# Optimization experiments

Measured on AMD Instinct MI355X. Metric: run time of the kernel, lower is better.

## Reference

```python
import jax, jax.numpy as jnp
import numpy as np

N_NEG = 60
TEMP = 0.07

def _normalize(x, axis):
    n = jnp.sqrt(jnp.sum(x * x, axis=axis, keepdims=True))
    return x / jnp.maximum(n, 1e-12)

def _grid_sample(img, grid):
    # img [B,C,H,W], grid [B,h,w,2] in [-1,1]; bilinear, padding_mode='border', align_corners=False
    B, C, H, W = img.shape
    ix = jnp.clip((grid[..., 0] + 1.0) * (W * 0.5) - 0.5, 0.0, W - 1.0)
    iy = jnp.clip((grid[..., 1] + 1.0) * (H * 0.5) - 0.5, 0.0, H - 1.0)
    x0 = jnp.floor(ix); y0 = jnp.floor(iy)
    x1 = jnp.minimum(x0 + 1.0, W - 1.0); y1 = jnp.minimum(y0 + 1.0, H - 1.0)
    wx = (ix - x0)[:, None]; wy = (iy - y0)[:, None]  # [B,1,h,w]
    imgf = img.reshape(B, C, H * W)
    hh, ww = grid.shape[1], grid.shape[2]
    def gat(yy, xx):
        idx = (yy * W + xx).astype(jnp.int32).reshape(B, 1, hh * ww)
        return jnp.take_along_axis(imgf, idx, axis=2).reshape(B, C, hh, ww)
    v00 = gat(y0, x0); v01 = gat(y0, x1); v10 = gat(y1, x0); v11 = gat(y1, x1)
    return (v00 * (1 - wx) * (1 - wy) + v01 * wx * (1 - wy)
            + v10 * (1 - wx) * wy + v11 * wx * wy)

def _forward(ref_fms, tgt_fms, target_l, target_r, queue):
    b, c, h, w = ref_fms.shape
    s = target_l.shape[-1] // w  # integer downscale factor (nearest interpolate == strided slice)
    disps_l = target_l[:, :, ::s, ::s] / float(s)   # [b,1,h,w]
    disps_r = target_r[:, :, ::s, ::s] / float(s)
    xb = jnp.broadcast_to(jnp.linspace(0.0, 1.0, w), (b, h, w))
    yb = jnp.broadcast_to(jnp.linspace(0.0, 1.0, h)[:, None], (b, h, w))

    def warp(img, disp):
        g = jnp.stack([xb + disp[:, 0] / w, yb], axis=-1)
        return _grid_sample(img, 2.0 * g - 1.0)

    # occlusion / validity mask (detached in the original)
    index = jnp.broadcast_to(jnp.arange(w, dtype=ref_fms.dtype), (b, 1, h, w))
    l2r2l = warp(warp(index, disps_r), -disps_l)
    masko = jnp.abs(index - l2r2l)[:, 0] < 3.0
    mask = masko & (disps_l[:, 0] > 0.0) & (xb - disps_l[:, 0] / w >= 0.0)
    mask = jax.lax.stop_gradient(mask).astype(ref_fms.dtype)  # [b,h,w]

    query = _normalize(ref_fms, 1)
    # positive: warp right feature to left view via disparity
    gpos = jnp.stack([xb - disps_l[:, 0] / w, yb], axis=-1)
    positive = _normalize(_grid_sample(tgt_fms, 2.0 * gpos - 1.0), 1)
    l_pos = jnp.einsum('bchw,bchw->bhw', query, positive)[..., None]

    # negatives: random integer pixel shifts around positive location
    # (no n_neg-fold repeat of tgt_fms; vmap grid_sample over the n axis instead)
    k1, k2 = jax.random.split(jax.random.key(1234))
    mag = jax.random.randint(k1, (b, h, w, N_NEG), 1, 25).astype(ref_fms.dtype)
    sgn = jnp.sign(jax.random.uniform(k2, (b, h, w, N_NEG)) - 0.5).astype(ref_fms.dtype)
    x_right = (xb - disps_l[:, 0] / w) * w
    fx = jnp.mod(x_right[..., None] + mag * sgn, float(w)) / w
    fy = fx / h  # faithful to original code (y coord reuses the normalized x coord)
    grids = jnp.moveaxis(jnp.stack([fx, fy], axis=-1), 3, 0)  # [n,b,h,w,2]
    neg = jax.vmap(lambda g: _grid_sample(tgt_fms, 2.0 * g - 1.0))(grids)  # [n,b,c,h,w]
    neg = _normalize(jnp.moveaxis(neg, 0, -1), 1)  # [b,c,h,w,n]
    l_neg = jnp.einsum('bchw,bchwn->bhwn', query, neg)

    qn = _normalize(queue, 0)  # forward re-normalizes the queue each call
    l_q = jnp.einsum('bchw,ck->bhwk', query, jax.lax.stop_gradient(qn))

    logits = jnp.concatenate([l_pos, l_neg, l_q], axis=-1) * mask[..., None]
    logits = logits.reshape(b * h * w, -1) / TEMP
    # CrossEntropyLoss with all-zero labels (positive is class 0)
    return jnp.mean(-jax.nn.log_softmax(logits, axis=-1)[:, 0])

def setup_inputs():
    key = jax.random.key(0)
    k1, k2, k3, k4, k5 = jax.random.split(key, 5)
    b, c, h, w = 2, 128, 64, 128
    H, W = 4 * h, 4 * w
    return {
        'ref_fms': jax.random.normal(k1, (b, c, h, w), jnp.float32),
        'tgt_fms': jax.random.normal(k2, (b, c, h, w), jnp.float32),
        'target_l': jax.random.uniform(k3, (b, 1, H, W), jnp.float32) * 64.0,
        'target_r': jax.random.uniform(k4, (b, 1, H, W), jnp.float32) * 64.0,
        'queue': jax.random.normal(k5, (c, 6000), jnp.float32),
    }

def reference(ref_fms, tgt_fms, target_l, target_r, queue):
    return _forward(ref_fms, tgt_fms, target_l, target_r, queue)
```

## Files before the change

### kernel.cpp

```cpp
#include <hip/hip_runtime.h>
#include <stdint.h>
#include <math.h>

#define HFM 64
#define WFM 128
#define CFM 128
#define BN 2
#define HWFM (HFM*WFM)
#define NPIX (BN*HWFM)
#define KQ 6000
#define KQP 6144
#define NNEG 60
#define NE (NPIX*NNEG)
#define EHALF_U 491520u
#define MSHIFT 15.0f
#define LOG2E 1.4426950408889634f
#define BSTRIDE 136

typedef _Float16 f16_8 __attribute__((ext_vector_type(8)));
typedef _Float16 f16_2 __attribute__((ext_vector_type(2)));
typedef float f32_4 __attribute__((ext_vector_type(4)));

__host__ __device__ __forceinline__ void threefry2x32(uint32_t k0, uint32_t k1,
                                                      uint32_t x0, uint32_t x1,
                                                      uint32_t* o0, uint32_t* o1) {
  uint32_t ks2 = k0 ^ k1 ^ 0x1BD11BDAu;
  x0 += k0; x1 += k1;
#define TFR(r) { x0 += x1; x1 = (x1 << (r)) | (x1 >> (32 - (r))); x1 ^= x0; }
  TFR(13) TFR(15) TFR(26) TFR(6)
  x0 += k1;  x1 += ks2 + 1u;
  TFR(17) TFR(29) TFR(16) TFR(24)
  x0 += ks2; x1 += k0 + 2u;
  TFR(13) TFR(15) TFR(26) TFR(6)
  x0 += k0;  x1 += k1 + 3u;
  TFR(17) TFR(29) TFR(16) TFR(24)
  x0 += k1;  x1 += ks2 + 4u;
  TFR(13) TFR(15) TFR(26) TFR(6)
  x0 += ks2; x1 += k0 + 5u;
#undef TFR
  *o0 = x0; *o1 = x1;
}

__device__ __forceinline__ void gs_coord(float t, float halfdim, float maxc,
                                         int* i0, int* i1, float* w) {
  float g = 2.0f * t - 1.0f;
  float x = (g + 1.0f) * halfdim - 0.5f;
  x = fminf(fmaxf(x, 0.0f), maxc);
  float f = floorf(x);
  *i0 = (int)f;
  *w = x - f;
  *i1 = (int)fminf(f + 1.0f, maxc);
}

__global__ __launch_bounds__(256) void k_A(
    const float* __restrict__ ref, const float* __restrict__ tgt,
    const float* __restrict__ queue,
    const float* __restrict__ target_l, const float* __restrict__ target_r,
    _Float16* __restrict__ refTf, _Float16* __restrict__ tgtTf,
    _Float16* __restrict__ queueTf, float2* __restrict__ qeb,
    float* __restrict__ maskArr, float* __restrict__ xr) {
  __shared__ float tile[32][33];
  int blk = blockIdx.x;
  int tid = threadIdx.x;
  if (blk < 64) {
    int p = blk * 256 + tid;
    int b = p >> 13;
    int rem = p & (HWFM - 1);
    int i = rem >> 7, j = rem & 127;
    const float stepx = 1.0f / 127.0f, stepy = 1.0f / 63.0f;
    float xb = (j == 127) ? 1.0f : j * stepx;
    float yb = (i == 63) ? 1.0f : i * stepy;
    const float* tl = target_l + (size_t)b * 256 * 512;
    const float* tr = target_r + (size_t)b * 256 * 512;
    float dl = tl[(4 * i) * 512 + 4 * j] * 0.25f;
    int y0i, y1i; float wy;
    gs_coord(yb, 32.0f, 63.0f, &y0i, &y1i, &wy);
    float t = xb - dl * (1.0f / 128.0f);
    int x0i, x1i; float wx;
    gs_coord(t, 64.0f, 127.0f, &x0i, &x1i, &wx);
    auto innerv = [&](int y, int x) -> float {
      float xbx = (x == 127) ? 1.0f : x * stepx;
      float drv = tr[(4 * y) * 512 + 4 * x] * 0.25f;
      float ti = xbx + drv * (1.0f / 128.0f);
      float g = 2.0f * ti - 1.0f;
      float ix2 = fminf(fmaxf((g + 1.0f) * 64.0f - 0.5f, 0.0f), 127.0f);
      float x0f = floorf(ix2);
      float wxp = ix2 - x0f;
      float x1f = fminf(x0f + 1.0f, 127.0f);
      return x0f * (1.0f - wxp) + x1f * wxp;
    };
    float v00 = innerv(y0i, x0i), v01 = innerv(y0i, x1i);
    float v10 = innerv(y1i, x0i), v11 = innerv(y1i, x1i);
    float l2r2l = v00 * (1.0f - wx) * (1.0f - wy) + v01 * wx * (1.0f - wy)
                + v10 * (1.0f - wx) * wy + v11 * wx * wy;
    bool masko = fabsf((float)j - l2r2l) < 3.0f;
    bool mk = masko && (dl > 0.0f) && (t >= 0.0f);
    maskArr[p] = mk ? 1.0f : 0.0f;
    xr[p] = t * 128.0f;
  } else if (blk < 88) {
    int k = (blk - 64) * 256 + tid;
    if (k < KQP) {
      if (k >= KQ) { qeb[k] = make_float2(0.0f, -1000.0f); }
      else {
        float ss = 0.0f;
        for (int c = 0; c < CFM; c++) { float v = queue[c * KQ + k]; ss += v * v; }
        float qi = 1.0f / fmaxf(sqrtf(ss), 1e-12f);
        qeb[k] = make_float2(qi * (LOG2E / 0.07f), -MSHIFT * LOG2E);
      }
    }
  } else if (blk < 856) {
    int q = blk - 88;
    int cy = q / 192, nx = q - cy * 192;
    int n0 = nx * 32, c0 = cy * 32;
    int tx = tid & 31, ty = tid >> 5;
#pragma unroll
    for (int i = 0; i < 32; i += 8) {
      int n = n0 + tx;
      tile[ty + i][tx] = (n < KQ) ? queue[(size_t)(c0 + ty + i) * KQ + n] : 0.0f;
    }
    __syncthreads();
#pragma unroll
    for (int i = 0; i < 32; i += 8)
      queueTf[(size_t)(n0 + ty + i) * CFM + (c0 + tx)] = (_Float16)tile[tx][ty + i];
  } else {
    int fblk = blk - 856;
    int z = fblk >> 10, yb_ = (fblk >> 8) & 3, xb_ = fblk & 255;
    int arr = z >> 1, b = z & 1;
    const float* src = (arr == 0 ? ref : tgt) + (size_t)b * CFM * HWFM;
    _Float16* dst = (arr == 0 ? refTf : tgtTf) + (size_t)b * HWFM * CFM;
    int x0 = xb_ * 32, y0 = yb_ * 32;
    int tx = tid & 31, ty = tid >> 5;
#pragma unroll
    for (int i = 0; i < 32; i += 8)
      tile[ty + i][tx] = src[(size_t)(y0 + ty + i) * HWFM + x0 + tx];
    __syncthreads();
#pragma unroll
    for (int i = 0; i < 32; i += 8)
      dst[(size_t)(x0 + ty + i) * CFM + (y0 + tx)] = (_Float16)tile[tx][ty + i];
  }
}

__global__ __launch_bounds__(256) void k_B(
    const _Float16* __restrict__ refTf, const _Float16* __restrict__ tgtTf,
    _Float16* __restrict__ QTf, float* __restrict__ stats,
    const float* __restrict__ maskArr, const float* __restrict__ xr,
    float* __restrict__ S, float* __restrict__ logit0,
    int* __restrict__ count, int* __restrict__ list) {
  __shared__ int wsum[4];
  int blk = blockIdx.x;
  int tid = threadIdx.x;
  int lane = tid & 63;
  if (blk == 0) {
    int wave = tid >> 6;
    int base_p = tid * 64;
    unsigned long long bits = 0ull;
    const float4* m4 = (const float4*)(maskArr + base_p);
#pragma unroll
    for (int k = 0; k < 16; k++) {
      float4 v = m4[k];
      if (v.x > 0.0f) bits |= 1ull << (4 * k + 0);
      if (v.y > 0.0f) bits |= 1ull << (4 * k + 1);
      if (v.z > 0.0f) bits |= 1ull << (4 * k + 2);
      if (v.w > 0.0f) bits |= 1ull << (4 * k + 3);
    }
    int m = __popcll(bits);
    int scan = m;
#pragma unroll
    for (int off = 1; off < 64; off <<= 1) {
      int n = __shfl_up(scan, off, 64);
      if (lane >= off) scan += n;
    }
    if (lane == 63) wsum[wave] = scan;
    __syncthreads();
    int wbase = 0;
    for (int w = 0; w < wave; w++) wbase += wsum[w];
    int idx = wbase + scan - m;
    for (int k = 0; k < 64; k++) {
      if ((bits >> k) & 1ull) list[idx++] = base_p + k;
    }
    if (tid == 255) *count = idx;
  } else if (blk < 65) {
    int sub = tid >> 6;
    int xg = (blk - 1) * 4 + sub;
    int b = xg >> 7, x = xg & 127;
    int xp = min(x + 1, 127);
    int c2 = lane * 2;
    int base = b * HWFM;
    f16_2 c0  = *(const f16_2*)(tgtTf + (size_t)(base + x) * CFM + c2);
    f16_2 c1  = *(const f16_2*)(tgtTf + (size_t)(base + WFM + x) * CFM + c2);
    f16_2 c0p = *(const f16_2*)(tgtTf + (size_t)(base + xp) * CFM + c2);
    f16_2 c1p = *(const f16_2*)(tgtTf + (size_t)(base + WFM + xp) * CFM + c2);
    float a0 = (float)c0[0], a1 = (float)c0[1];
    float b0 = (float)c1[0], b1 = (float)c1[1];
    float p0 = (float)c0p[0], p1 = (float)c0p[1];
    float q0 = (float)c1p[0], q1 = (float)c1p[1];
    float s[7];
    s[0] = a0 * a0 + a1 * a1;
    s[1] = a0 * b0 + a1 * b1;
    s[2] = b0 * b0 + b1 * b1;
    s[3] = a0 * p0 + a1 * p1;
    s[4] = a0 * q0 + a1 * q1;
    s[5] = b0 * p0 + b1 * p1;
    s[6] = b0 * q0 + b1 * q1;
#pragma unroll
    for (int o = 32; o; o >>= 1)
#pragma unroll
      for (int k = 0; k < 7; k++) s[k] += __shfl_xor(s[k], o, 64);
    if (lane == 0) {
      float* st = stats + (size_t)xg * 8;
#pragma unroll
      for (int k = 0; k < 7; k++) st[k] = s[k];
      st[7] = 0.0f;
    }
  } else {
    int wave = tid >> 6;
    int p = (blk - 65) * 4 + wave;
    float mk = maskArr[p];
    if (mk == 0.0f) return;
    int b = p >> 13;
    int rem = p & (HWFM - 1);
    int i = rem >> 7;
    const float stepy = 1.0f / 63.0f;
    float yb = (i == 63) ? 1.0f : i * stepy;
    float t = xr[p] * (1.0f / 128.0f);
    int y0i, y1i; float wy;
    gs_coord(yb, 32.0f, 63.0f, &y0i, &y1i, &wy);
    int x0i, x1i; float wx;
    gs_coord(t, 64.0f, 127.0f, &x0i, &x1i, &wx);

    int c2 = lane * 2;
    f16_2 q2 = *(const f16_2*)(refTf + (size_t)p * CFM + c2);
    int bo = b * HWFM;
    f16_2 a2 = *(const f16_2*)(tgtTf + (size_t)(bo + y0i * WFM + x0i) * CFM + c2);
    f16_2 b2 = *(const f16_2*)(tgtTf + (size_t)(bo + y0i * WFM + x1i) * CFM + c2);
    f16_2 cc2 = *(const f16_2*)(tgtTf + (size_t)(bo + y1i * WFM + x0i) * CFM + c2);
    f16_2 d2 = *(const f16_2*)(tgtTf + (size_t)(bo + y1i * WFM + x1i) * CFM + c2);

    float w00 = (1.0f - wx) * (1.0f - wy), w01 = wx * (1.0f - wy);
    float w10 = (1.0f - wx) * wy,          w11 = wx * wy;
    float q0 = (float)q2[0], q1 = (float)q2[1];
    float v0 = w00 * (float)a2[0] + w01 * (float)b2[0] + w10 * (float)cc2[0] + w11 * (float)d2[0];
    float v1 = w00 * (float)a2[1] + w01 * (float)b2[1] + w10 * (float)cc2[1] + w11 * (float)d2[1];

    float s0 = q0 * q0 + q1 * q1;
    float s1 = q0 * v0 + q1 * v1;
    float s2 = v0 * v0 + v1 * v1;
#pragma unroll
    for (int o = 32; o; o >>= 1) {
      s0 += __shfl_xor(s0, o, 64);
      s1 += __shfl_xor(s1, o, 64);
      s2 += __shfl_xor(s2, o, 64);
    }
    float inv = 1.0f / fmaxf(sqrtf(s0), 1e-12f);
    f16_2 qw; qw[0] = (_Float16)(q0 * inv); qw[1] = (_Float16)(q1 * inv);
    *(f16_2*)(QTf + (size_t)p * CFM + c2) = qw;
    if (lane == 0) {
      float lpos = (s1 * inv) / fmaxf(sqrtf(s2), 1e-12f);
      float lg0 = lpos / 0.07f;
      logit0[p] = lg0;
      S[p] = expf(lg0 - MSHIFT);
    }
  }
}

__global__ __launch_bounds__(256) void k_gemm(
    const _Float16* __restrict__ QTf,
    const _Float16* __restrict__ queueTf,
    const _Float16* __restrict__ tgtTf,
    const float2* __restrict__ qeb,
    float* __restrict__ S, float* __restrict__ D,
    const int* __restrict__ count, const int* __restrict__ list) {
  __shared__ _Float16 Bs[2][128 * BSTRIDE];
  __shared__ float Srow[64];
  __shared__ int pb[64];
  int tid = threadIdx.x;
  int cnt = *count;
  int pblk = blockIdx.y * 64;
  if (pblk >= cnt) return;
  int wave = tid >> 6, lane = tid & 63;
  int quad = lane >> 4, l16 = lane & 15;
  int wm = wave >> 1, wn = wave & 1;

  if (tid < 64) {
    Srow[tid] = 0.0f;
    pb[tid] = list[min(pblk + tid, cnt - 1)] >> 13;
  }

  f16_8 Af[2][4];
  int r0 = pblk + wm * 32;
#pragma unroll
  for (int mt = 0; mt < 2; mt++) {
    int prow = list[min(r0 + mt * 16 + l16, cnt - 1)];
    const _Float16* arow = QTf + (size_t)prow * CFM + quad * 8;
#pragma unroll
    for (int ks = 0; ks < 4; ks++)
      Af[mt][ks] = *(const f16_8*)(arow + ks * 32);
  }

  f16_8 sreg[8];
  int srow[8], sc16[8];
#pragma unroll
  for (int it = 0; it < 8; it++) {
    int idx = it * 256 + tid;
    srow[it] = idx >> 4; sc16[it] = idx & 15;
  }
  auto load_src = [&](const _Float16* bsrc) {
#pragma unroll
    for (int it = 0; it < 8; it++)
      sreg[it] = *(const f16_8*)(bsrc + (size_t)srow[it] * CFM + sc16[it] * 8);
  };
  auto write_lds = [&](int buf) {
#pragma unroll
    for (int it = 0; it < 8; it++)
      *(f16_8*)(&Bs[buf][srow[it] * BSTRIDE + sc16[it] * 8]) = sreg[it];
  };

  int nbase = blockIdx.x * 8 * 128;
  int cur;
  float rowsum[2][4] = {{0.0f,0.0f,0.0f,0.0f},{0.0f,0.0f,0.0f,0.0f}};

  if (blockIdx.x < 4) {
    int batch = blockIdx.x >> 1;
    load_src(tgtTf + ((size_t)batch * HWFM + (blockIdx.x & 1) * 128) * CFM);
    write_lds(0);
    __syncthreads();
    load_src(queueTf + (size_t)nbase * CFM);
    f32_4 acc[2][4];
#pragma unroll
    for (int mt = 0; mt < 2; mt++)
#pragma unroll
      for (int nt = 0; nt < 4; nt++)
        acc[mt][nt] = (f32_4){0.0f, 0.0f, 0.0f, 0.0f};
#pragma unroll
    for (int ks = 0; ks < 4; ks++) {
      f16_8 Bk[4];
#pragma unroll
      for (int nt = 0; nt < 4; nt++)
        Bk[nt] = *(const f16_8*)(&Bs[0][(wn * 64 + nt * 16 + l16) * BSTRIDE + ks * 32 + quad * 8]);
#pragma unroll
      for (int mt = 0; mt < 2; mt++)
#pragma unroll
        for (int nt = 0; nt < 4; nt++)
          acc[mt][nt] = __builtin_amdgcn_mfma_f32_16x16x32_f16(Af[mt][ks], Bk[nt], acc[mt][nt], 0, 0, 0);
    }
#pragma unroll
    for (int mt = 0; mt < 2; mt++)
#pragma unroll
      for (int nt = 0; nt < 4; nt++)
#pragma unroll
        for (int r = 0; r < 4; r++) {
          int rowloc = wm * 32 + mt * 16 + quad * 4 + r;
          int slot = pblk + rowloc;
          int colL = (blockIdx.x & 1) * 128 + wn * 64 + nt * 16 + l16;
          if (slot < cnt && pb[rowloc] == batch)
            D[(size_t)slot * 256 + colL] = acc[mt][nt][r];
        }
    write_lds(1);
    __syncthreads();
    cur = 1;
  } else {
    load_src(queueTf + (size_t)nbase * CFM);
    write_lds(0);
    __syncthreads();
    cur = 0;
  }

#pragma unroll
  for (int ic = 0; ic < 8; ic++) {
    int n0 = nbase + ic * 128;
    if (ic + 1 < 8) load_src(queueTf + (size_t)(n0 + 128) * CFM);
    float2 qb[4];
#pragma unroll
    for (int nt = 0; nt < 4; nt++) qb[nt] = qeb[n0 + wn * 64 + nt * 16 + l16];

    f32_4 acc[2][4];
#pragma unroll
    for (int mt = 0; mt < 2; mt++)
#pragma unroll
      for (int nt = 0; nt < 4; nt++)
        acc[mt][nt] = (f32_4){0.0f, 0.0f, 0.0f, 0.0f};
#pragma unroll
    for (int ks = 0; ks < 4; ks++) {
      f16_8 Bk[4];
#pragma unroll
      for (int nt = 0; nt < 4; nt++)
        Bk[nt] = *(const f16_8*)(&Bs[cur][(wn * 64 + nt * 16 + l16) * BSTRIDE + ks * 32 + quad * 8]);
#pragma unroll
      for (int mt = 0; mt < 2; mt++)
#pragma unroll
        for (int nt = 0; nt < 4; nt++)
          acc[mt][nt] = __builtin_amdgcn_mfma_f32_16x16x32_f16(Af[mt][ks], Bk[nt], acc[mt][nt], 0, 0, 0);
    }
    if (ic + 1 < 8) write_lds(cur ^ 1);

#pragma unroll
    for (int nt = 0; nt < 4; nt++)
#pragma unroll
      for (int mt = 0; mt < 2; mt++)
#pragma unroll
        for (int r = 0; r < 4; r++)
          rowsum[mt][r] += exp2f(fmaf(acc[mt][nt][r], qb[nt].x, qb[nt].y));
    __syncthreads();
    cur ^= 1;
  }

#pragma unroll
  for (int mt = 0; mt < 2; mt++)
#pragma unroll
    for (int r = 0; r < 4; r++) {
      float vv = rowsum[mt][r];
      vv += __shfl_xor(vv, 1);
      vv += __shfl_xor(vv, 2);
      vv += __shfl_xor(vv, 4);
      vv += __shfl_xor(vv, 8);
      rowsum[mt][r] = vv;
    }
  if (l16 == 0) {
#pragma unroll
    for (int mt = 0; mt < 2; mt++)
#pragma unroll
      for (int r = 0; r < 4; r++)
        atomicAdd(&Srow[wm * 32 + mt * 16 + quad * 4 + r], rowsum[mt][r]);
  }
  __syncthreads();
  if (tid < 64) {
    int pr = pblk + tid;
    if (pr < cnt) atomicAdd(&S[list[pr]], Srow[tid]);
  }
}

__global__ __launch_bounds__(256) void k_negatives_lite(
    const float* __restrict__ D, const float* __restrict__ stats,
    const float* __restrict__ xr, float* __restrict__ S,
    const int* __restrict__ count, const int* __restrict__ list,
    uint32_t k1a, uint32_t k1b, uint32_t k2a, uint32_t k2b) {
  int tid = threadIdx.x;
  int wave = tid >> 6, lane = tid & 63;
  int cnt = *count;
  int slot = blockIdx.x * 4 + wave;
  if (slot >= cnt) return;
  int p = list[slot];
  int b = p >> 13;
  float esum = 0.0f;
  if (lane < NNEG) {
    uint32_t e = (uint32_t)(p * NNEG + lane);
    uint32_t h0, h1;
    threefry2x32(k1a, k1b, e, e + (uint32_t)NE, &h0, &h1);
    uint32_t off = ((h0 % 24u) * 16u + (h1 % 24u)) % 24u;
    float mag = (float)(1u + off);
    uint32_t ub;
    {
      uint32_t a, bm;
      if (e < EHALF_U) { threefry2x32(k2a, k2b, e, e + EHALF_U, &a, &bm); ub = a; }
      else             { threefry2x32(k2a, k2b, e - EHALF_U, e, &a, &bm); ub = bm; }
    }
    float u = __uint_as_float((ub >> 9) | 0x3F800000u) - 1.0f;
    float sg = (u > 0.5f) ? 1.0f : ((u < 0.5f) ? -1.0f : 0.0f);

    float v = xr[p] + mag * sg;
    float r = fmodf(v, 128.0f);
    if (r < 0.0f) r += 128.0f;
    float fx = r * (1.0f / 128.0f);
    float fy = fx * (1.0f / 64.0f);
    int x0i, x1i, y0i, y1i; float wx, wy;
    gs_coord(fx, 64.0f, 127.0f, &x0i, &x1i, &wx);
    gs_coord(fy, 32.0f, 63.0f, &y0i, &y1i, &wy);

    const float* Dp = D + (size_t)slot * 256;
    float d00 = Dp[x0i], d01 = Dp[x1i];
    float d10 = Dp[128 + x0i], d11 = Dp[128 + x1i];
    float u0 = 1.0f - wy, u1 = wy;
    float dv0 = u0 * d00 + u1 * d10;
    float dv1 = u0 * d01 + u1 * d11;
    float dot = (1.0f - wx) * dv0 + wx * dv1;

    const float* st0 = stats + (size_t)(b * 128 + x0i) * 8;
    const float* st1 = stats + (size_t)(b * 128 + x1i) * 8;
    float4 sa = *(const float4*)st0;
    float4 sb = *(const float4*)(st0 + 4);
    float4 sc = *(const float4*)st1;
    float a0 = u0 * u0, a1 = u0 * u1, a2 = u1 * u1;
    float nB0 = a0 * sa.x + 2.0f * a1 * sa.y + a2 * sa.z;
    float nB1 = a0 * sc.x + 2.0f * a1 * sc.y + a2 * sc.z;
    float cB  = a0 * sa.w + a1 * (sb.x + sb.y) + a2 * sb.z;
    float wx0 = 1.0f - wx;
    float nsq = wx0 * wx0 * nB0 + 2.0f * wx * wx0 * cB + wx * wx * nB1;
    float ln = dot / fmaxf(sqrtf(fmaxf(nsq, 0.0f)), 1e-12f);
    esum = __expf(ln * (1.0f / 0.07f) - MSHIFT);
  }
#pragma unroll
  for (int o = 32; o; o >>= 1) esum += __shfl_xor(esum, o, 64);
  if (lane == 0) atomicAdd(&S[p], esum);
}

__global__ __launch_bounds__(1024) void k_finalize(
    const float* __restrict__ S, const float* __restrict__ logit0,
    const float* __restrict__ maskArr, float* __restrict__ out) {
  int tid = threadIdx.x;
  const float cmask = logf(6061.0f);
  double acc = 0.0;
  for (int p = tid; p < NPIX; p += 1024) {
    float term = (maskArr[p] > 0.0f) ? (logf(S[p]) + MSHIFT - logit0[p]) : cmask;
    acc += (double)term;
  }
#pragma unroll
  for (int off = 32; off; off >>= 1) acc += __shfl_down(acc, off, 64);
  __shared__ double sd[16];
  if ((tid & 63) == 0) sd[tid >> 6] = acc;
  __syncthreads();
  if (tid == 0) {
    double tot = 0.0;
    for (int w = 0; w < 16; w++) tot += sd[w];
    out[0] = (float)(tot / (double)NPIX);
  }
}

extern "C" void kernel_launch(void* const* d_in, const int* in_sizes, int n_in,
                              void* d_out, int out_size, void* d_ws, size_t ws_size,
                              hipStream_t stream) {
  const float* ref   = (const float*)d_in[0];
  const float* tgt   = (const float*)d_in[1];
  const float* tl    = (const float*)d_in[2];
  const float* tr    = (const float*)d_in[3];
  const float* queue = (const float*)d_in[4];
  float* out = (float*)d_out;
  float* ws = (float*)d_ws;

  float2* qeb = (float2*)ws;
  float* S    = ws + 12288;
  float* lg0  = ws + 28672;
  float* mk   = ws + 45056;
  float* xr   = ws + 61440;
  int* count  = (int*)(ws + 77824);
  int* list   = (int*)(ws + 77840);
  _Float16* QTf     = (_Float16*)(ws + 94464);
  _Float16* queueTf = (_Float16*)(ws + 1143040);
  _Float16* tgtTf   = (_Float16*)(ws + 1536256);
  _Float16* refTf   = (_Float16*)(ws + 2584832);
  float* stats = ws + 3633408;
  float* D     = ws + 3635456;

  uint32_t b0o0, b0o1, b1o0, b1o1;
  threefry2x32(0u, 1234u, 0u, 2u, &b0o0, &b0o1);
  threefry2x32(0u, 1234u, 1u, 3u, &b1o0, &b1o1);
  uint32_t k1a = b0o0, k1b = b1o0, k2a = b0o1, k2b = b1o1;

  k_A<<<dim3(4952), dim3(256), 0, stream>>>(ref, tgt, queue, tl, tr,
                                            refTf, tgtTf, queueTf, qeb, mk, xr);
  k_B<<<dim3(65 + 4096), dim3(256), 0, stream>>>(refTf, tgtTf, QTf, stats,
                                                 mk, xr, S, lg0, count, list);
  k_gemm<<<dim3(6, NPIX / 64), dim3(256), 0, stream>>>(QTf, queueTf, tgtTf, qeb,
                                                       S, D, count, list);
  k_negatives_lite<<<dim3(NPIX / 4), dim3(256), 0, stream>>>(D, stats, xr, S, count, list,
                                                             k1a, k1b, k2a, k2b);
  k_finalize<<<dim3(1), dim3(1024), 0, stream>>>(S, lg0, mk, out);
}
```

Measured before the change: 131.9 us.

## Use direct global-to-LDS loads with XOR swizzle, larger GEMM M tile, vectorized transposes

The GEMM kernel now stages queue and target tiles with global_load_lds straight into LDS, using an XOR swizzle in place of row padding. This removes the register round-trip for staging. The M tile per block doubles to 128 rows, with 4x4 MFMA accumulators per wave and a launch-bounds occupancy hint. The transpose/fp16 conversion blocks in k_A are rewritten to read float4 and write 8-wide fp16 vectors over 64-channel tiles. The larger tile raises register pressure and halves the number of GEMM blocks, which may hurt latency hiding when few pixels are active.

```diff
diff --git a/kernel.cpp b/kernel.cpp
--- a/kernel.cpp
+++ b/kernel.cpp
@@ -15,7 +15,6 @@
 #define EHALF_U 491520u
 #define MSHIFT 15.0f
 #define LOG2E 1.4426950408889634f
-#define BSTRIDE 136
 
 typedef _Float16 f16_8 __attribute__((ext_vector_type(8)));
 typedef _Float16 f16_2 __attribute__((ext_vector_type(2)));
@@ -59,7 +58,7 @@
     _Float16* __restrict__ refTf, _Float16* __restrict__ tgtTf,
     _Float16* __restrict__ queueTf, float2* __restrict__ qeb,
     float* __restrict__ maskArr, float* __restrict__ xr) {
-  __shared__ float tile[32][33];
+  __shared__ float tile[64][35];
   int blk = blockIdx.x;
   int tid = threadIdx.x;
   if (blk < 64) {
@@ -108,35 +107,55 @@
         qeb[k] = make_float2(qi * (LOG2E / 0.07f), -MSHIFT * LOG2E);
       }
     }
-  } else if (blk < 856) {
+  } else if (blk < 472) {
     int q = blk - 88;
     int cy = q / 192, nx = q - cy * 192;
-    int n0 = nx * 32, c0 = cy * 32;
-    int tx = tid & 31, ty = tid >> 5;
-#pragma unroll
-    for (int i = 0; i < 32; i += 8) {
-      int n = n0 + tx;
-      tile[ty + i][tx] = (n < KQ) ? queue[(size_t)(c0 + ty + i) * KQ + n] : 0.0f;
-    }
-    __syncthreads();
-#pragma unroll
-    for (int i = 0; i < 32; i += 8)
-      queueTf[(size_t)(n0 + ty + i) * CFM + (c0 + tx)] = (_Float16)tile[tx][ty + i];
+    int n0 = nx * 32, c0 = cy * 64;
+    int c = tid >> 2, qq = tid & 3;
+    const float* sp = queue + (size_t)(c0 + c) * KQ + n0 + qq * 4;
+    if (n0 + 32 <= KQ) {
+      float4 v0 = *(const float4*)sp;
+      float4 v1 = *(const float4*)(sp + 16);
+      tile[c][qq * 4 + 0] = v0.x; tile[c][qq * 4 + 1] = v0.y;
+      tile[c][qq * 4 + 2] = v0.z; tile[c][qq * 4 + 3] = v0.w;
+      tile[c][qq * 4 + 16] = v1.x; tile[c][qq * 4 + 17] = v1.y;
+      tile[c][qq * 4 + 18] = v1.z; tile[c][qq * 4 + 19] = v1.w;
+    } else {
+#pragma unroll
+      for (int k = 0; k < 4; k++) {
+        int n = n0 + qq * 4 + k;
+        tile[c][qq * 4 + k] = (n < KQ) ? sp[k] : 0.0f;
+        tile[c][qq * 4 + 16 + k] = (n + 16 < KQ) ? sp[16 + k] : 0.0f;
+      }
+    }
+    __syncthreads();
+    int x = tid >> 3, j8 = tid & 7;
+    f16_8 o;
+#pragma unroll
+    for (int k = 0; k < 8; k++) o[k] = (_Float16)tile[j8 * 8 + k][x];
+    *(f16_8*)(queueTf + (size_t)(n0 + x) * CFM + c0 + j8 * 8) = o;
   } else {
-    int fblk = blk - 856;
-    int z = fblk >> 10, yb_ = (fblk >> 8) & 3, xb_ = fblk & 255;
+    int fblk = blk - 472;
+    int z = fblk >> 9, rem2 = fblk & 511;
+    int cy = rem2 >> 8, xt = rem2 & 255;
+    int x0 = xt * 32, c0 = cy * 64;
     int arr = z >> 1, b = z & 1;
     const float* src = (arr == 0 ? ref : tgt) + (size_t)b * CFM * HWFM;
     _Float16* dst = (arr == 0 ? refTf : tgtTf) + (size_t)b * HWFM * CFM;
-    int x0 = xb_ * 32, y0 = yb_ * 32;
-    int tx = tid & 31, ty = tid >> 5;
-#pragma unroll
-    for (int i = 0; i < 32; i += 8)
-      tile[ty + i][tx] = src[(size_t)(y0 + ty + i) * HWFM + x0 + tx];
-    __syncthreads();
-#pragma unroll
-    for (int i = 0; i < 32; i += 8)
-      dst[(size_t)(x0 + ty + i) * CFM + (y0 + tx)] = (_Float16)tile[tx][ty + i];
+    int c = tid >> 2, qq = tid & 3;
+    const float* sp = src + (size_t)(c0 + c) * HWFM + x0 + qq * 4;
+    float4 v0 = *(const float4*)sp;
+    float4 v1 = *(const float4*)(sp + 16);
+    tile[c][qq * 4 + 0] = v0.x; tile[c][qq * 4 + 1] = v0.y;
+    tile[c][qq * 4 + 2] = v0.z; tile[c][qq * 4 + 3] = v0.w;
+    tile[c][qq * 4 + 16] = v1.x; tile[c][qq * 4 + 17] = v1.y;
+    tile[c][qq * 4 + 18] = v1.z; tile[c][qq * 4 + 19] = v1.w;
+    __syncthreads();
+    int x = tid >> 3, j8 = tid & 7;
+    f16_8 o;
+#pragma unroll
+    for (int k = 0; k < 8; k++) o[k] = (_Float16)tile[j8 * 8 + k][x];
+    *(f16_8*)(dst + (size_t)(x0 + x) * CFM + c0 + j8 * 8) = o;
   }
 }
 
@@ -263,33 +282,33 @@
   }
 }
 
-__global__ __launch_bounds__(256) void k_gemm(
+__global__ __launch_bounds__(256, 2) void k_gemm(
     const _Float16* __restrict__ QTf,
     const _Float16* __restrict__ queueTf,
     const _Float16* __restrict__ tgtTf,
     const float2* __restrict__ qeb,
     float* __restrict__ S, float* __restrict__ D,
     const int* __restrict__ count, const int* __restrict__ list) {
-  __shared__ _Float16 Bs[2][128 * BSTRIDE];
-  __shared__ float Srow[64];
-  __shared__ int pb[64];
+  __shared__ _Float16 Bs[2][128 * CFM];
+  __shared__ float Srow[128];
+  __shared__ int pb[128];
   int tid = threadIdx.x;
   int cnt = *count;
-  int pblk = blockIdx.y * 64;
+  int pblk = blockIdx.y * 128;
   if (pblk >= cnt) return;
   int wave = tid >> 6, lane = tid & 63;
   int quad = lane >> 4, l16 = lane & 15;
   int wm = wave >> 1, wn = wave & 1;
 
-  if (tid < 64) {
+  if (tid < 128) {
     Srow[tid] = 0.0f;
     pb[tid] = list[min(pblk + tid, cnt - 1)] >> 13;
   }
 
-  f16_8 Af[2][4];
-  int r0 = pblk + wm * 32;
-#pragma unroll
-  for (int mt = 0; mt < 2; mt++) {
+  f16_8 Af[4][4];
+  int r0 = pblk + wm * 64;
+#pragma unroll
+  for (int mt = 0; mt < 4; mt++) {
     int prow = list[min(r0 + mt * 16 + l16, cnt - 1)];
     const _Float16* arow = QTf + (size_t)prow * CFM + quad * 8;
 #pragma unroll
@@ -297,37 +316,32 @@
       Af[mt][ks] = *(const f16_8*)(arow + ks * 32);
   }
 
-  f16_8 sreg[8];
-  int srow[8], sc16[8];
-#pragma unroll
-  for (int it = 0; it < 8; it++) {
-    int idx = it * 256 + tid;
-    srow[it] = idx >> 4; sc16[it] = idx & 15;
-  }
-  auto load_src = [&](const _Float16* bsrc) {
-#pragma unroll
-    for (int it = 0; it < 8; it++)
-      sreg[it] = *(const f16_8*)(bsrc + (size_t)srow[it] * CFM + sc16[it] * 8);
-  };
-  auto write_lds = [&](int buf) {
-#pragma unroll
-    for (int it = 0; it < 8; it++)
-      *(f16_8*)(&Bs[buf][srow[it] * BSTRIDE + sc16[it] * 8]) = sreg[it];
+  int lrow = lane >> 4, lchunk = lane & 15;
+  auto stage = [&](const _Float16* bsrc, int buf) {
+#pragma unroll
+    for (int i = 0; i < 8; i++) {
+      int rb = wave * 32 + i * 4;
+      int r = rb + lrow;
+      const _Float16* g = bsrc + (size_t)r * CFM + ((lchunk ^ (r & 7)) << 3);
+      __builtin_amdgcn_global_load_lds(
+          (const __attribute__((address_space(1))) void*)g,
+          (__attribute__((address_space(3))) void*)(&Bs[buf][rb * CFM]),
+          16, 0, 0);
+    }
   };
 
   int nbase = blockIdx.x * 8 * 128;
   int cur;
-  float rowsum[2][4] = {{0.0f,0.0f,0.0f,0.0f},{0.0f,0.0f,0.0f,0.0f}};
+  float rowsum[4][4] = {{0,0,0,0},{0,0,0,0},{0,0,0,0},{0,0,0,0}};
 
   if (blockIdx.x < 4) {
     int batch = blockIdx.x >> 1;
-    load_src(tgtTf + ((size_t)batch * HWFM + (blockIdx.x & 1) * 128) * CFM);
-    write_lds(0);
-    __syncthreads();
-    load_src(queueTf + (size_t)nbase * CFM);
-    f32_4 acc[2][4];
-#pragma unroll
-    for (int mt = 0; mt < 2; mt++)
+    stage(tgtTf + ((size_t)batch * HWFM + (blockIdx.x & 1) * 128) * CFM, 0);
+    __syncthreads();
+    stage(queueTf + (size_t)nbase * CFM, 1);
+    f32_4 acc[4][4];
+#pragma unroll
+    for (int mt = 0; mt < 4; mt++)
 #pragma unroll
       for (int nt = 0; nt < 4; nt++)
         acc[mt][nt] = (f32_4){0.0f, 0.0f, 0.0f, 0.0f};
@@ -335,32 +349,32 @@
     for (int ks = 0; ks < 4; ks++) {
       f16_8 Bk[4];
 #pragma unroll
-      for (int nt = 0; nt < 4; nt++)
-        Bk[nt] = *(const f16_8*)(&Bs[0][(wn * 64 + nt * 16 + l16) * BSTRIDE + ks * 32 + quad * 8]);
-#pragma unroll
-      for (int mt = 0; mt < 2; mt++)
+      for (int nt = 0; nt < 4; nt++) {
+        int brow = wn * 64 + nt * 16 + l16;
+        Bk[nt] = *(const f16_8*)(&Bs[0][brow * CFM + ((ks * 32 + quad * 8) ^ ((brow & 7) * 8))]);
+      }
+#pragma unroll
+      for (int mt = 0; mt < 4; mt++)
 #pragma unroll
         for (int nt = 0; nt < 4; nt++)
           acc[mt][nt] = __builtin_amdgcn_mfma_f32_16x16x32_f16(Af[mt][ks], Bk[nt], acc[mt][nt], 0, 0, 0);
     }
 #pragma unroll
-    for (int mt = 0; mt < 2; mt++)
+    for (int mt = 0; mt < 4; mt++)
 #pragma unroll
       for (int nt = 0; nt < 4; nt++)
 #pragma unroll
         for (int r = 0; r < 4; r++) {
-          int rowloc = wm * 32 + mt * 16 + quad * 4 + r;
+          int rowloc = wm * 64 + mt * 16 + quad * 4 + r;
           int slot = pblk + rowloc;
           int colL = (blockIdx.x & 1) * 128 + wn * 64 + nt * 16 + l16;
           if (slot < cnt && pb[rowloc] == batch)
             D[(size_t)slot * 256 + colL] = acc[mt][nt][r];
         }
-    write_lds(1);
     __syncthreads();
     cur = 1;
   } else {
-    load_src(queueTf + (size_t)nbase * CFM);
-    write_lds(0);
+    stage(queueTf + (size_t)nbase * CFM, 0);
     __syncthreads();
     cur = 0;
   }
@@ -368,14 +382,14 @@
 #pragma unroll
   for (int ic = 0; ic < 8; ic++) {
     int n0 = nbase + ic * 128;
-    if (ic + 1 < 8) load_src(queueTf + (size_t)(n0 + 128) * CFM);
+    if (ic + 1 < 8) stage(queueTf + (size_t)(n0 + 128) * CFM, cur ^ 1);
     float2 qb[4];
 #pragma unroll
     for (int nt = 0; nt < 4; nt++) qb[nt] = qeb[n0 + wn * 64 + nt * 16 + l16];
 
-    f32_4 acc[2][4];
-#pragma unroll
-    for (int mt = 0; mt < 2; mt++)
+    f32_4 acc[4][4];
+#pragma unroll
+    for (int mt = 0; mt < 4; mt++)
 #pragma unroll
       for (int nt = 0; nt < 4; nt++)
         acc[mt][nt] = (f32_4){0.0f, 0.0f, 0.0f, 0.0f};
@@ -383,20 +397,21 @@
     for (int ks = 0; ks < 4; ks++) {
       f16_8 Bk[4];
 #pragma unroll
-      for (int nt = 0; nt < 4; nt++)
-        Bk[nt] = *(const f16_8*)(&Bs[cur][(wn * 64 + nt * 16 + l16) * BSTRIDE + ks * 32 + quad * 8]);
-#pragma unroll
-      for (int mt = 0; mt < 2; mt++)
+      for (int nt = 0; nt < 4; nt++) {
+        int brow = wn * 64 + nt * 16 + l16;
+        Bk[nt] = *(const f16_8*)(&Bs[cur][brow * CFM + ((ks * 32 + quad * 8) ^ ((brow & 7) * 8))]);
+      }
+#pragma unroll
+      for (int mt = 0; mt < 4; mt++)
 #pragma unroll
         for (int nt = 0; nt < 4; nt++)
           acc[mt][nt] = __builtin_amdgcn_mfma_f32_16x16x32_f16(Af[mt][ks], Bk[nt], acc[mt][nt], 0, 0, 0);
     }
-    if (ic + 1 < 8) write_lds(cur ^ 1);
 
 #pragma unroll
     for (int nt = 0; nt < 4; nt++)
 #pragma unroll
-      for (int mt = 0; mt < 2; mt++)
+      for (int mt = 0; mt < 4; mt++)
 #pragma unroll
         for (int r = 0; r < 4; r++)
           rowsum[mt][r] += exp2f(fmaf(acc[mt][nt][r], qb[nt].x, qb[nt].y));
@@ -405,7 +420,7 @@
   }
 
 #pragma unroll
-  for (int mt = 0; mt < 2; mt++)
+  for (int mt = 0; mt < 4; mt++)
 #pragma unroll
     for (int r = 0; r < 4; r++) {
       float vv = rowsum[mt][r];
@@ -417,13 +432,13 @@
     }
   if (l16 == 0) {
 #pragma unroll
-    for (int mt = 0; mt < 2; mt++)
+    for (int mt = 0; mt < 4; mt++)
 #pragma unroll
       for (int r = 0; r < 4; r++)
-        atomicAdd(&Srow[wm * 32 + mt * 16 + quad * 4 + r], rowsum[mt][r]);
+        atomicAdd(&Srow[wm * 64 + mt * 16 + quad * 4 + r], rowsum[mt][r]);
   }
   __syncthreads();
-  if (tid < 64) {
+  if (tid < 128) {
     int pr = pblk + tid;
     if (pr < cnt) atomicAdd(&S[list[pr]], Srow[tid]);
   }
@@ -545,12 +560,12 @@
   threefry2x32(0u, 1234u, 1u, 3u, &b1o0, &b1o1);
   uint32_t k1a = b0o0, k1b = b1o0, k2a = b0o1, k2b = b1o1;
 
-  k_A<<<dim3(4952), dim3(256), 0, stream>>>(ref, tgt, queue, tl, tr,
+  k_A<<<dim3(2520), dim3(256), 0, stream>>>(ref, tgt, queue, tl, tr,
                                             refTf, tgtTf, queueTf, qeb, mk, xr);
   k_B<<<dim3(65 + 4096), dim3(256), 0, stream>>>(refTf, tgtTf, QTf, stats,
                                                  mk, xr, S, lg0, count, list);
-  k_gemm<<<dim3(6, NPIX / 64), dim3(256), 0, stream>>>(QTf, queueTf, tgtTf, qeb,
-                                                       S, D, count, list);
+  k_gemm<<<dim3(6, NPIX / 128), dim3(256), 0, stream>>>(QTf, queueTf, tgtTf, qeb,
+                                                        S, D, count, list);
   k_negatives_lite<<<dim3(NPIX / 4), dim3(256), 0, stream>>>(D, stats, xr, S, count, list,
                                                              k1a, k1b, k2a, k2b);
   k_finalize<<<dim3(1), dim3(1024), 0, stream>>>(S, lg0, mk, out);
```

Measured after the change: 135.7 us. +2.8%, slower.
